# Performance work log

Hardware: AMD Instinct MI355X
Metric: run time of the kernel (lower is better)

Reference implementation:

```python
import jax, jax.numpy as jnp
import numpy as np

B, QS, FD = 16384, 1204, 7
N_CHUNKS, N_OFFSETS, WIN = 120, 5, 10


def setup_inputs() -> dict:
    key = jax.random.key(0)
    ks = jax.random.split(key, 10)
    s = 0.05
    return {
        "x": jax.random.normal(ks[0], (B, QS, FD), dtype=jnp.float32),
        "w_step": jax.random.normal(ks[1], (FD,), dtype=jnp.float32) * s,
        "b_step": jax.random.normal(ks[2], (), dtype=jnp.float32) * s,
        "wA": jax.random.normal(ks[3], (600, 128), dtype=jnp.float32) * s,
        "bA": jax.random.normal(ks[4], (128,), dtype=jnp.float32) * s,
        "wB": jax.random.normal(ks[5], (128, 32), dtype=jnp.float32) * s,
        "bB": jax.random.normal(ks[6], (32,), dtype=jnp.float32) * s,
        "wC": jax.random.normal(ks[7], (32, 2), dtype=jnp.float32) * s,
        "bC": jax.random.normal(ks[8], (2,), dtype=jnp.float32) * s,
    }


def reference(x, w_step, b_step, wA, bA, wB, bB, wC, bC):
    # fc_step: (b, qs, 7) -> (b, qs)
    out = jnp.einsum('bqf,f->bq', x, w_step) + b_step
    # Windowed max: starts[i, o] = o + i*10, window of size 10.
    starts = jnp.arange(N_CHUNKS)[:, None] * WIN + jnp.arange(N_OFFSETS)[None, :]  # (120, 5)
    idx = starts[..., None] + jnp.arange(WIN)  # (120, 5, 10)
    pooled = out[:, idx].max(axis=-1)  # (b, 120, 5)
    cat = pooled.reshape(x.shape[0], N_CHUNKS * N_OFFSETS)  # (b, 600)
    h = jax.nn.relu(cat @ wA + bA)
    h = jax.nn.relu(h @ wB + bB)
    return h @ wC + bC
```

## Files before the change

### kernel.cpp

```cpp
#include <hip/hip_runtime.h>

#define NB      16384
#define QS      1204
#define FD      7
#define ROWF    (QS * FD)
#define ROWF4   (ROWF / 4)
#define NCH     120
#define NOFF    5
#define WINSZ   10
#define CATN    600
#define H1N     128
#define H2N     32
#define OUTN    2
#define G       8
#define NTHR    256

__global__ __launch_bounds__(NTHR) void fused_struct3(
    const float* __restrict__ x,
    const float* __restrict__ w_step,
    const float* __restrict__ b_step,
    const float* __restrict__ wA,
    const float* __restrict__ bA,
    const float* __restrict__ wB,
    const float* __restrict__ bB,
    const float* __restrict__ wC,
    const float* __restrict__ bC,
    float* __restrict__ out)
{
    __shared__ __align__(16) float rowbuf[ROWF];
    __shared__ float orow[QS];
    __shared__ __align__(16) float cat_s[G][CATN];
    __shared__ __align__(16) float h1_s[G][H1N];
    __shared__ float h2_s[G][H2N];

    const int t  = threadIdx.x;
    const int b0 = blockIdx.x * G;

    const float w0 = w_step[0], w1 = w_step[1], w2 = w_step[2], w3 = w_step[3],
                w4 = w_step[4], w5 = w_step[5], w6 = w_step[6];
    const float bs = b_step[0];

    for (int g = 0; g < G; ++g) {
        const float4* src = (const float4*)(x + (size_t)(b0 + g) * ROWF);
        float4* dst = (float4*)rowbuf;
        #pragma unroll
        for (int i = 0; i < 9; ++i) {
            int idx = t + i * NTHR;
            if (idx < ROWF4) dst[idx] = src[idx];
        }
        __syncthreads();

        for (int q = t; q < QS; q += NTHR) {
            const float* p = rowbuf + q * FD;
            float s = fmaf(p[0], w0, bs);
            s = fmaf(p[1], w1, s);
            s = fmaf(p[2], w2, s);
            s = fmaf(p[3], w3, s);
            s = fmaf(p[4], w4, s);
            s = fmaf(p[5], w5, s);
            s = fmaf(p[6], w6, s);
            orow[q] = s;
        }
        __syncthreads();

        for (int j = t; j < CATN; j += NTHR) {
            int ci = j / NOFF;
            int o  = j - ci * NOFF;
            int st = ci * WINSZ + o;
            float m = orow[st];
            #pragma unroll
            for (int w = 1; w < WINSZ; ++w) m = fmaxf(m, orow[st + w]);
            cat_s[g][j] = m;
        }
        __syncthreads();
    }

    {
        const int n  = t & (H1N - 1);
        const int g0 = (t >> 7) << 2;
        float acc0 = 0.f, acc1 = 0.f, acc2 = 0.f, acc3 = 0.f;
        for (int k = 0; k < CATN; k += 4) {
            const float4 c0 = *(const float4*)&cat_s[g0 + 0][k];
            const float4 c1 = *(const float4*)&cat_s[g0 + 1][k];
            const float4 c2 = *(const float4*)&cat_s[g0 + 2][k];
            const float4 c3 = *(const float4*)&cat_s[g0 + 3][k];
            const float a0 = wA[(k + 0) * H1N + n];
            const float a1 = wA[(k + 1) * H1N + n];
            const float a2 = wA[(k + 2) * H1N + n];
            const float a3 = wA[(k + 3) * H1N + n];
            acc0 = fmaf(c0.x, a0, acc0); acc0 = fmaf(c0.y, a1, acc0);
            acc0 = fmaf(c0.z, a2, acc0); acc0 = fmaf(c0.w, a3, acc0);
            acc1 = fmaf(c1.x, a0, acc1); acc1 = fmaf(c1.y, a1, acc1);
            acc1 = fmaf(c1.z, a2, acc1); acc1 = fmaf(c1.w, a3, acc1);
            acc2 = fmaf(c2.x, a0, acc2); acc2 = fmaf(c2.y, a1, acc2);
            acc2 = fmaf(c2.z, a2, acc2); acc2 = fmaf(c2.w, a3, acc2);
            acc3 = fmaf(c3.x, a0, acc3); acc3 = fmaf(c3.y, a1, acc3);
            acc3 = fmaf(c3.z, a2, acc3); acc3 = fmaf(c3.w, a3, acc3);
        }
        const float bias = bA[n];
        h1_s[g0 + 0][n] = fmaxf(acc0 + bias, 0.f);
        h1_s[g0 + 1][n] = fmaxf(acc1 + bias, 0.f);
        h1_s[g0 + 2][n] = fmaxf(acc2 + bias, 0.f);
        h1_s[g0 + 3][n] = fmaxf(acc3 + bias, 0.f);
    }
    __syncthreads();

    {
        const int g  = t >> 5;
        const int n2 = t & 31;
        float acc = bB[n2];
        #pragma unroll 4
        for (int k = 0; k < H1N; ++k)
            acc = fmaf(h1_s[g][k], wB[k * H2N + n2], acc);
        h2_s[g][n2] = fmaxf(acc, 0.f);
    }
    __syncthreads();

    if (t < G * OUTN) {
        const int g = t >> 1;
        const int c = t & 1;
        float acc = bC[c];
        #pragma unroll
        for (int k = 0; k < H2N; ++k)
            acc = fmaf(h2_s[g][k], wC[k * OUTN + c], acc);
        out[(size_t)(b0 + g) * OUTN + c] = acc;
    }
}

extern "C" void kernel_launch(void* const* d_in, const int* in_sizes, int n_in,
                              void* d_out, int out_size, void* d_ws, size_t ws_size,
                              hipStream_t stream) {
    const float* x      = (const float*)d_in[0];
    const float* w_step = (const float*)d_in[1];
    const float* b_step = (const float*)d_in[2];
    const float* wA     = (const float*)d_in[3];
    const float* bA     = (const float*)d_in[4];
    const float* wB     = (const float*)d_in[5];
    const float* bB     = (const float*)d_in[6];
    const float* wC     = (const float*)d_in[7];
    const float* bC     = (const float*)d_in[8];
    float* out = (float*)d_out;

    dim3 grid(NB / G);
    fused_struct3<<<grid, NTHR, 0, stream>>>(
        x, w_step, b_step, wA, bA, wB, bB, wC, bC, out);
}
```

Baseline: 820.9 us.

## Process one row per wavefront directly from global memory and split layer-1 K

Drops the per-row shared-memory staging of x and the serial loop over 8 rows. Each of the 4 wavefronts now computes the fc_step dot products for its own row, reading the 7-float groups straight from global memory. The group size is halved to 4 rows per block, doubling the grid. The first dense layer is re-tiled so each thread computes 4 outputs with float4 wA loads over half of K, followed by a shared-memory reduction. This removes barrier serialization but uses strided, uncoalesced 7-float global loads, and wA is re-read per block twice as often.

```diff
diff --git a/kernel.cpp b/kernel.cpp
--- a/kernel.cpp
+++ b/kernel.cpp
@@ -4,7 +4,6 @@
 #define QS      1204
 #define FD      7
 #define ROWF    (QS * FD)
-#define ROWF4   (ROWF / 4)
 #define NCH     120
 #define NOFF    5
 #define WINSZ   10
@@ -12,7 +11,7 @@
 #define H1N     128
 #define H2N     32
 #define OUTN    2
-#define G       8
+#define G       4
 #define NTHR    256
 
 __global__ __launch_bounds__(NTHR) void fused_struct3(
@@ -27,31 +26,24 @@
     const float* __restrict__ bC,
     float* __restrict__ out)
 {
-    __shared__ __align__(16) float rowbuf[ROWF];
-    __shared__ float orow[QS];
+    __shared__ __align__(16) float orow_s[G][QS];
     __shared__ __align__(16) float cat_s[G][CATN];
     __shared__ __align__(16) float h1_s[G][H1N];
-    __shared__ float h2_s[G][H2N];
+    __shared__ __align__(16) float h2_s[G][H2N];
 
-    const int t  = threadIdx.x;
-    const int b0 = blockIdx.x * G;
+    const int t    = threadIdx.x;
+    const int lane = t & 63;
+    const int w    = t >> 6;
+    const int b0   = blockIdx.x * G;
 
     const float w0 = w_step[0], w1 = w_step[1], w2 = w_step[2], w3 = w_step[3],
                 w4 = w_step[4], w5 = w_step[5], w6 = w_step[6];
     const float bs = b_step[0];
 
-    for (int g = 0; g < G; ++g) {
-        const float4* src = (const float4*)(x + (size_t)(b0 + g) * ROWF);
-        float4* dst = (float4*)rowbuf;
-        #pragma unroll
-        for (int i = 0; i < 9; ++i) {
-            int idx = t + i * NTHR;
-            if (idx < ROWF4) dst[idx] = src[idx];
-        }
-        __syncthreads();
-
-        for (int q = t; q < QS; q += NTHR) {
-            const float* p = rowbuf + q * FD;
+    {
+        const float* row = x + (size_t)(b0 + w) * ROWF;
+        for (int q = lane; q < QS; q += 64) {
+            const float* p = row + q * FD;
             float s = fmaf(p[0], w0, bs);
             s = fmaf(p[1], w1, s);
             s = fmaf(p[2], w2, s);
@@ -59,60 +51,66 @@
             s = fmaf(p[4], w4, s);
             s = fmaf(p[5], w5, s);
             s = fmaf(p[6], w6, s);
-            orow[q] = s;
+            orow_s[w][q] = s;
         }
-        __syncthreads();
-
-        for (int j = t; j < CATN; j += NTHR) {
-            int ci = j / NOFF;
-            int o  = j - ci * NOFF;
-            int st = ci * WINSZ + o;
-            float m = orow[st];
-            #pragma unroll
-            for (int w = 1; w < WINSZ; ++w) m = fmaxf(m, orow[st + w]);
-            cat_s[g][j] = m;
-        }
-        __syncthreads();
-    }
-
-    {
-        const int n  = t & (H1N - 1);
-        const int g0 = (t >> 7) << 2;
-        float acc0 = 0.f, acc1 = 0.f, acc2 = 0.f, acc3 = 0.f;
-        for (int k = 0; k < CATN; k += 4) {
-            const float4 c0 = *(const float4*)&cat_s[g0 + 0][k];
-            const float4 c1 = *(const float4*)&cat_s[g0 + 1][k];
-            const float4 c2 = *(const float4*)&cat_s[g0 + 2][k];
-            const float4 c3 = *(const float4*)&cat_s[g0 + 3][k];
-            const float a0 = wA[(k + 0) * H1N + n];
-            const float a1 = wA[(k + 1) * H1N + n];
-            const float a2 = wA[(k + 2) * H1N + n];
-            const float a3 = wA[(k + 3) * H1N + n];
-            acc0 = fmaf(c0.x, a0, acc0); acc0 = fmaf(c0.y, a1, acc0);
-            acc0 = fmaf(c0.z, a2, acc0); acc0 = fmaf(c0.w, a3, acc0);
-            acc1 = fmaf(c1.x, a0, acc1); acc1 = fmaf(c1.y, a1, acc1);
-            acc1 = fmaf(c1.z, a2, acc1); acc1 = fmaf(c1.w, a3, acc1);
-            acc2 = fmaf(c2.x, a0, acc2); acc2 = fmaf(c2.y, a1, acc2);
-            acc2 = fmaf(c2.z, a2, acc2); acc2 = fmaf(c2.w, a3, acc2);
-            acc3 = fmaf(c3.x, a0, acc3); acc3 = fmaf(c3.y, a1, acc3);
-            acc3 = fmaf(c3.z, a2, acc3); acc3 = fmaf(c3.w, a3, acc3);
-        }
-        const float bias = bA[n];
-        h1_s[g0 + 0][n] = fmaxf(acc0 + bias, 0.f);
-        h1_s[g0 + 1][n] = fmaxf(acc1 + bias, 0.f);
-        h1_s[g0 + 2][n] = fmaxf(acc2 + bias, 0.f);
-        h1_s[g0 + 3][n] = fmaxf(acc3 + bias, 0.f);
     }
     __syncthreads();
 
+    for (int j = t; j < G * CATN; j += NTHR) {
+        int g  = j / CATN;
+        int jj = j - g * CATN;
+        int ci = jj / NOFF;
+        int o  = jj - ci * NOFF;
+        int st = ci * WINSZ + o;
+        float m = orow_s[g][st];
+        #pragma unroll
+        for (int u = 1; u < WINSZ; ++u) m = fmaxf(m, orow_s[g][st + u]);
+        cat_s[g][jj] = m;
+    }
+    __syncthreads();
+
+    float4* red = (float4*)&orow_s[0][0];
     {
+        const int c4 = t & 31;
+        const int g  = (t >> 5) & 3;
+        const int kh = t >> 7;
+        const int k0 = kh * (CATN / 2);
+        const float* wAp = wA + (size_t)k0 * H1N + 4 * c4;
+        const float* cp  = &cat_s[g][k0];
+        float4 acc = make_float4(0.f, 0.f, 0.f, 0.f);
+        #pragma unroll 4
+        for (int k = 0; k < CATN / 2; ++k) {
+            const float4 a = *(const float4*)(wAp + (size_t)k * H1N);
+            const float  c = cp[k];
+            acc.x = fmaf(c, a.x, acc.x);
+            acc.y = fmaf(c, a.y, acc.y);
+            acc.z = fmaf(c, a.z, acc.z);
+            acc.w = fmaf(c, a.w, acc.w);
+        }
+        red[t] = acc;
+    }
+    __syncthreads();
+    if (t < 128) {
+        const int c4 = t & 31;
         const int g  = t >> 5;
-        const int n2 = t & 31;
-        float acc = bB[n2];
-        #pragma unroll 4
+        const float4 a = red[t];
+        const float4 b = red[t + 128];
+        const float4 bias = *(const float4*)(bA + 4 * c4);
+        h1_s[g][4 * c4 + 0] = fmaxf(a.x + b.x + bias.x, 0.f);
+        h1_s[g][4 * c4 + 1] = fmaxf(a.y + b.y + bias.y, 0.f);
+        h1_s[g][4 * c4 + 2] = fmaxf(a.z + b.z + bias.z, 0.f);
+        h1_s[g][4 * c4 + 3] = fmaxf(a.w + b.w + bias.w, 0.f);
+    }
+    __syncthreads();
+
+    if (t < G * H2N) {
+        const int g = t >> 5;
+        const int n = t & 31;
+        float acc = bB[n];
+        #pragma unroll 8
         for (int k = 0; k < H1N; ++k)
-            acc = fmaf(h1_s[g][k], wB[k * H2N + n2], acc);
-        h2_s[g][n2] = fmaxf(acc, 0.f);
+            acc = fmaf(h1_s[g][k], wB[k * H2N + n], acc);
+        h2_s[g][n] = fmaxf(acc, 0.f);
     }
     __syncthreads();
 
```

New measurement: 852.8 us. 3.9% more time.
